# Kernel optimization log

Hardware: AMD Instinct MI355X
Metric: run time of the kernel (lower is better)

Reference implementation:

```python
import jax, jax.numpy as jnp
import numpy as np

NUM_PTS = 8   # num_points_per_face
K = 5         # self.k


def _sq_dist(x, y):
    # squared euclidean distance matrix (Nx, Ny); matches torch.cdist**2 / sum((a-b)**2)
    x2 = jnp.sum(x * x, axis=1)[:, None]
    y2 = jnp.sum(y * y, axis=1)[None, :]
    d = x2 + y2 - 2.0 * (x @ y.T)
    return jnp.maximum(d, 0.0)


def setup_inputs() -> dict:
    key = jax.random.key(0)
    k1, k2, k3, k4, k5, k6, k7 = jax.random.split(key, 7)
    V, Fs, Ft = 2048, 4096, 4096
    return {
        "source_vertices": jax.random.normal(k1, (1, V, 3), dtype=jnp.float32),
        "source_faces": jax.random.randint(k2, (Fs, 3), 0, V),
        "target_vertices": jax.random.normal(k3, (1, V, 3), dtype=jnp.float32),
        "target_faces": jax.random.randint(k4, (3, Ft), 0, V),
        "face_probs": jax.random.uniform(k5, (Fs,), dtype=jnp.float32),
        "r1u": jax.random.uniform(k6, (Fs, NUM_PTS), dtype=jnp.float32),
        "r2u": jax.random.uniform(k7, (Fs, NUM_PTS), dtype=jnp.float32),
    }


def reference(source_vertices, source_faces, target_vertices, target_faces, face_probs, r1u, r2u):
    sv = source_vertices[0]                 # (V, 3)
    tv = target_vertices[0]                 # (V, 3)
    tf = target_faces.T                     # (Ft, 3)
    Fs = source_faces.shape[0]

    src_bc = sv[source_faces].mean(axis=1)  # (Fs, 3) source barycenters
    tgt_bc = tv[tf].mean(axis=1)            # (Ft, 3) target barycenters

    # ---- forward loss: prob-weighted min squared distance to target barycenters
    d_fwd = _sq_dist(src_bc, tgt_bc)        # (Fs, Ft)
    forward_loss = jnp.sum(face_probs * jnp.min(d_fwd, axis=1))

    # ---- sample points from triangles via barycentric coords
    r1 = jnp.sqrt(r1u)
    w1 = 1.0 - r1
    w2 = r1 * (1.0 - r2u)
    w3 = r1 * r2u
    v1 = sv[source_faces[:, 0]]             # (Fs, 3)
    v2 = sv[source_faces[:, 1]]
    v3 = sv[source_faces[:, 2]]
    pts = (w1[..., None] * v1[:, None] + w2[..., None] * v2[:, None]
           + w3[..., None] * v3[:, None]).reshape(-1, 3)   # (P, 3), P = Fs*NUM_PTS
    pt_faces = jnp.repeat(jnp.arange(Fs), NUM_PTS)          # (P,)
    pt_probs = face_probs[pt_faces]                         # (P,)

    # ---- reverse loss, batched over all P points
    d_src = _sq_dist(pts, src_bc)                           # (P, Fs)
    neg_d, idx = jax.lax.top_k(-d_src, K + 1)               # K+1 smallest distances
    tri_dists = -neg_d                                      # (P, K+1)
    mask = idx != pt_faces[:, None]                         # exclude own face
    has_self = jnp.any(~mask, axis=1)
    excl_pos = jnp.where(has_self, jnp.argmin(mask, axis=1), K + 1)  # (P,)
    t = jnp.arange(K)
    sel = t[None, :] + (t[None, :] >= excl_pos[:, None]).astype(jnp.int32)  # (P, K)
    valid_dists = jnp.take_along_axis(tri_dists, sel, axis=1)   # (P, K)
    valid_idx = jnp.take_along_axis(idx, sel, axis=1)           # (P, K)
    valid_probs = face_probs[valid_idx]                         # (P, K)

    min_tgt = jnp.min(_sq_dist(pts, tgt_bc), axis=1)            # (P,)

    reverse_loss = jnp.sum(pt_probs * min_tgt
                           + (1.0 - pt_probs) * jnp.mean(valid_probs * valid_dists, axis=1))
    return forward_loss + reverse_loss
```

## Files before the change

### kernel.cpp

```cpp
#include <hip/hip_runtime.h>
#include <math.h>

#define FS 4096
#define FT 4096
#define TS 256
#define NPH 16
#define REVB 2048
#define BIGF 3.0e38f
#define KEYINF 0xFFFFFFFFu

typedef float v2f __attribute__((ext_vector_type(2)));

__device__ __forceinline__ unsigned umin32(unsigned a, unsigned b) { return a < b ? a : b; }
__device__ __forceinline__ unsigned umax32(unsigned a, unsigned b) { return a < b ? b : a; }

__device__ __forceinline__ unsigned med3u(unsigned a, unsigned b, unsigned c) {
    unsigned d;
    asm("v_med3_u32 %0, %1, %2, %3" : "=v"(d) : "v"(a), "v"(b), "v"(c));
    return d;
}

__device__ __forceinline__ unsigned and_or(unsigned a, unsigned m, unsigned o) {
    unsigned d;
    asm("v_and_or_b32 %0, %1, %2, %3" : "=v"(d) : "v"(a), "v"(m), "v"(o));
    return d;
}

__device__ __forceinline__ v2f pk_add(v2f a, v2f b) {
    v2f d;
    asm("v_pk_add_f32 %0, %1, %2" : "=v"(d) : "v"(a), "v"(b));
    return d;
}
__device__ __forceinline__ v2f pk_fma(v2f a, v2f b, v2f c) {
    v2f d;
    asm("v_pk_fma_f32 %0, %1, %2, %3" : "=v"(d) : "v"(a), "v"(b), "v"(c));
    return d;
}
__device__ __forceinline__ void pk_fma_acc(v2f& d, v2f a, v2f b) {
    asm("v_pk_fma_f32 %0, %1, %2, %0" : "+v"(d) : "v"(a), "v"(b));
}

__device__ __forceinline__ void gl_lds16(const float4* g, float4* l) {
    __builtin_amdgcn_global_load_lds(
        (__attribute__((address_space(1))) void*)(g),
        (__attribute__((address_space(3))) void*)(l), 16, 0, 0);
}

__device__ __forceinline__ float block_reduce_sum(float v) {
    __shared__ float s[8];
    for (int o = 32; o > 0; o >>= 1) v += __shfl_down(v, o, 64);
    int lane = threadIdx.x & 63, wid = threadIdx.x >> 6;
    if (lane == 0) s[wid] = v;
    __syncthreads();
    int nw = blockDim.x >> 6;
    v = (threadIdx.x < (unsigned)nw) ? s[threadIdx.x] : 0.f;
    if (wid == 0)
        for (int o = 4; o > 0; o >>= 1) v += __shfl_down(v, o, 64);
    return v;
}

#define CE(x, y) { unsigned _n = umin32(x, y); y = umax32(x, y); x = _n; }

__device__ __forceinline__ void merge32(unsigned s[6]) {
    #pragma unroll
    for (int m = 1; m <= 16; m <<= 1) {
        unsigned b0 = __shfl_xor(s[0], m, 64), b1 = __shfl_xor(s[1], m, 64);
        unsigned b2 = __shfl_xor(s[2], m, 64), b3 = __shfl_xor(s[3], m, 64);
        unsigned b4 = __shfl_xor(s[4], m, 64), b5 = __shfl_xor(s[5], m, 64);
        unsigned l0 = s[0], l1 = s[1];
        unsigned l2 = umin32(s[2], b5), l3 = umin32(s[3], b4);
        unsigned l4 = umin32(s[4], b3), l5 = umin32(s[5], b2);
        unsigned l6 = b1, l7 = b0;
        CE(l0, l4) CE(l1, l5) CE(l2, l6) CE(l3, l7)
        CE(l0, l2) CE(l1, l3) CE(l4, l6) CE(l5, l7)
        CE(l0, l1) CE(l2, l3) CE(l4, l5) CE(l6, l7)
        s[0] = l0; s[1] = l1; s[2] = l2; s[3] = l3; s[4] = l4; s[5] = l5;
    }
}

__global__ __launch_bounds__(64) void k_prep(
        const float* __restrict__ sv, const int* __restrict__ sf,
        const float* __restrict__ tv, const int* __restrict__ tf,
        float4* __restrict__ sbc2, float4* __restrict__ tbc2,
        float4* __restrict__ sbcr, float* __restrict__ out) {
    int i = blockIdx.x * 64 + threadIdx.x;
    if (i == 0) out[0] = 0.f;
    if (i >= FS) return;
    const float third = 1.f / 3.f;
    int a = sf[3*i], b = sf[3*i+1], c = sf[3*i+2];
    float x = (sv[3*a  ] + sv[3*b  ] + sv[3*c  ]) * third;
    float y = (sv[3*a+1] + sv[3*b+1] + sv[3*c+1]) * third;
    float z = (sv[3*a+2] + sv[3*b+2] + sv[3*c+2]) * third;
    float n2 = x*x + y*y + z*z;
    sbcr[i] = make_float4(x, y, z, n2);
    int ta = tf[i], tb = tf[FT + i], tc = tf[2*FT + i];
    float tx = (tv[3*ta  ] + tv[3*tb  ] + tv[3*tc  ]) * third;
    float ty = (tv[3*ta+1] + tv[3*tb+1] + tv[3*tc+1]) * third;
    float tz = (tv[3*ta+2] + tv[3*tb+2] + tv[3*tc+2]) * third;
    float tn2 = tx*tx + ty*ty + tz*tz;

    int tt = i >> 10, cc = i & 1023;
    int g = cc >> 6, half = (cc >> 5) & 1, pp = cc & 31;
    int lo4 = tt*1024 + g*32 + pp, hi4 = lo4 + 512;
    float* S = (float*)sbc2;
    S[4*lo4 + half]     = -2.f*x;  S[4*lo4 + 2 + half] = -2.f*y;
    S[4*hi4 + half]     = -2.f*z;  S[4*hi4 + 2 + half] = n2;
    float* T = (float*)tbc2;
    T[4*lo4 + half]     = -2.f*tx; T[4*lo4 + 2 + half] = -2.f*ty;
    T[4*hi4 + half]     = -2.f*tz; T[4*hi4 + 2 + half] = tn2;
}

__global__ __launch_bounds__(128, 4) void k_main(
        const float* __restrict__ sv, const int* __restrict__ sf,
        const float* __restrict__ fp,
        const float* __restrict__ r1u, const float* __restrict__ r2u,
        const float4* __restrict__ sbc2, const float4* __restrict__ tbc2,
        const float4* __restrict__ sbcr, float* __restrict__ out) {
    __shared__ float4 tileS[TS];
    __shared__ float4 tileT[TS];
    int tid  = threadIdx.x;
    int seg  = tid & 31;
    int slot = tid >> 5;
    float contrib = 0.f;

    if (blockIdx.x < REVB) {
        int pt0  = blockIdx.x * 16 + slot * 4;
        int face = pt0 >> 3;

        int a = sf[3*face], b = sf[3*face+1], c = sf[3*face+2];
        float ax = sv[3*a], ay = sv[3*a+1], az = sv[3*a+2];
        float bx = sv[3*b], by = sv[3*b+1], bz = sv[3*b+2];
        float cx = sv[3*c], cy = sv[3*c+1], cz = sv[3*c+2];
        float4 r14 = ((const float4*)r1u)[pt0 >> 2];
        float4 r24 = ((const float4*)r2u)[pt0 >> 2];
        v2f pxb[4], pyb[4], pzb[4], p2b[4];
        {
            float r1a[4] = {r14.x, r14.y, r14.z, r14.w};
            float r2a[4] = {r24.x, r24.y, r24.z, r24.w};
            #pragma unroll
            for (int i = 0; i < 4; ++i) {
                float r1 = sqrtf(r1a[i]);
                float w1 = 1.f - r1, w2 = r1 * (1.f - r2a[i]), w3 = r1 * r2a[i];
                float px = w1*ax + w2*bx + w3*cx;
                float py = w1*ay + w2*by + w3*cy;
                float pz = w1*az + w2*bz + w3*cz;
                float p2 = px*px + py*py + pz*pz;
                pxb[i] = (v2f){px, px}; pyb[i] = (v2f){py, py};
                pzb[i] = (v2f){pz, pz}; p2b[i] = (v2f){p2, p2};
            }
        }

        unsigned s0[4], s1[4], s2[4];
        #pragma unroll
        for (int i = 0; i < 4; ++i) { s0[i]=KEYINF; s1[i]=KEYINF; s2[i]=KEYINF; }
        v2f vm2[4];
        #pragma unroll
        for (int i = 0; i < 4; ++i) vm2[i] = (v2f){BIGF, BIGF};

        unsigned kMask = 0xFFFFF000u;

        for (int p = 0; p < NPH; ++p) {
            int b0 = ((p >> 2) << 10) + ((p & 3) << 7);
            __syncthreads();
            gl_lds16(&sbc2[b0 + tid],       &tileS[tid]);
            gl_lds16(&sbc2[b0 + 512 + tid], &tileS[128 + tid]);
            gl_lds16(&tbc2[b0 + tid],       &tileT[tid]);
            gl_lds16(&tbc2[b0 + 512 + tid], &tileT[128 + tid]);
            __syncthreads();
            unsigned jja = (unsigned)(p * TS + seg);
            #pragma unroll
            for (int jp = 0; jp < 4; ++jp) {
                float4 lo = tileS[(jp << 5) + seg];
                float4 hi = tileS[128 + (jp << 5) + seg];
                v2f cx2 = {lo.x, lo.y}, cy2 = {lo.z, lo.w};
                v2f cz2 = {hi.x, hi.y}, cw2 = {hi.z, hi.w};
                #pragma unroll
                for (int i = 0; i < 4; ++i) {
                    v2f d2 = pk_add(cw2, p2b[i]);
                    pk_fma_acc(d2, pzb[i], cz2);
                    pk_fma_acc(d2, pyb[i], cy2);
                    pk_fma_acc(d2, pxb[i], cx2);
                    unsigned ka = and_or(__float_as_uint(d2.x), kMask, jja);
                    unsigned kb = and_or(__float_as_uint(d2.y), kMask, jja + 32u);
                    unsigned n0 = umin32(s0[i], ka);
                    unsigned n1 = med3u(s0[i], s1[i], ka);
                    unsigned n2 = med3u(s1[i], s2[i], ka);
                    s0[i]=n0; s1[i]=n1; s2[i]=n2;
                    n0 = umin32(s0[i], kb);
                    n1 = med3u(s0[i], s1[i], kb);
                    n2 = med3u(s1[i], s2[i], kb);
                    s0[i]=n0; s1[i]=n1; s2[i]=n2;
                }
                jja += 64;
            }
            #pragma unroll
            for (int jp = 0; jp < 4; ++jp) {
                float4 lo = tileT[(jp << 5) + seg];
                float4 hi = tileT[128 + (jp << 5) + seg];
                v2f cx2 = {lo.x, lo.y}, cy2 = {lo.z, lo.w};
                v2f cz2 = {hi.x, hi.y}, cw2 = {hi.z, hi.w};
                #pragma unroll
                for (int i = 0; i < 4; ++i) {
                    v2f t = pk_fma(pzb[i], cz2, cw2);
                    pk_fma_acc(t, pyb[i], cy2);
                    pk_fma_acc(t, pxb[i], cx2);
                    vm2[i].x = fminf(vm2[i].x, t.x);
                    vm2[i].y = fminf(vm2[i].y, t.y);
                }
            }
        }

        float vm[4];
        #pragma unroll
        for (int i = 0; i < 4; ++i) {
            float v = fminf(vm2[i].x, vm2[i].y);
            v = fminf(v, __shfl_xor(v, 1, 64));
            v = fminf(v, __shfl_xor(v, 2, 64));
            v = fminf(v, __shfl_xor(v, 4, 64));
            v = fminf(v, __shfl_xor(v, 8, 64));
            v = fminf(v, __shfl_xor(v, 16, 64));
            vm[i] = v;
        }

        float pf = fp[face];
        float csum = 0.f;
        #pragma unroll
        for (int i = 0; i < 4; ++i) {
            unsigned srt[6] = {s0[i], s1[i], s2[i], KEYINF, KEYINF, KEYINF};
            merge32(srt);
            if (seg == 0) {
                int   q0 = srt[0] & 0xFFF, q1 = srt[1] & 0xFFF, q2 = srt[2] & 0xFFF;
                int   q3 = srt[3] & 0xFFF, q4 = srt[4] & 0xFFF, q5 = srt[5] & 0xFFF;
                float d0 = __uint_as_float(srt[0] & 0xFFFFF000u);
                float d1 = __uint_as_float(srt[1] & 0xFFFFF000u);
                float d2 = __uint_as_float(srt[2] & 0xFFFFF000u);
                float d3 = __uint_as_float(srt[3] & 0xFFFFF000u);
                float d4 = __uint_as_float(srt[4] & 0xFFFFF000u);
                float d5 = __uint_as_float(srt[5] & 0xFFFFF000u);

                int skip = 5;
                if      (q0 == face) skip = 0;
                else if (q1 == face) skip = 1;
                else if (q2 == face) skip = 2;
                else if (q3 == face) skip = 3;
                else if (q4 == face) skip = 4;

                float s = 0.f;
                if (skip != 0) s += fp[q0] * d0;
                if (skip != 1) s += fp[q1] * d1;
                if (skip != 2) s += fp[q2] * d2;
                if (skip != 3) s += fp[q3] * d3;
                if (skip != 4) s += fp[q4] * d4;
                if (skip != 5) s += fp[q5] * d5;

                float mtd = fmaxf(vm[i] + p2b[i].x, 0.f);
                csum += pf * mtd + (1.f - pf) * (s * 0.2f);
            }
        }
        if (seg == 0) contrib = csum;
    } else {
        int f0 = (blockIdx.x - REVB) * 16 + slot * 4;
        float qw[4];
        v2f qxb[4], qyb[4], qzb[4];
        #pragma unroll
        for (int i = 0; i < 4; ++i) {
            float4 q = sbcr[f0 + i];
            qxb[i] = (v2f){q.x, q.x}; qyb[i] = (v2f){q.y, q.y};
            qzb[i] = (v2f){q.z, q.z}; qw[i] = q.w;
        }
        v2f vf2[4];
        #pragma unroll
        for (int i = 0; i < 4; ++i) vf2[i] = (v2f){BIGF, BIGF};

        for (int p = 0; p < NPH; ++p) {
            int b0 = ((p >> 2) << 10) + ((p & 3) << 7);
            __syncthreads();
            gl_lds16(&tbc2[b0 + tid],       &tileT[tid]);
            gl_lds16(&tbc2[b0 + 512 + tid], &tileT[128 + tid]);
            __syncthreads();
            #pragma unroll
            for (int jp = 0; jp < 4; ++jp) {
                float4 lo = tileT[(jp << 5) + seg];
                float4 hi = tileT[128 + (jp << 5) + seg];
                v2f cx2 = {lo.x, lo.y}, cy2 = {lo.z, lo.w};
                v2f cz2 = {hi.x, hi.y}, cw2 = {hi.z, hi.w};
                #pragma unroll
                for (int i = 0; i < 4; ++i) {
                    v2f t = pk_fma(qzb[i], cz2, cw2);
                    pk_fma_acc(t, qyb[i], cy2);
                    pk_fma_acc(t, qxb[i], cx2);
                    vf2[i].x = fminf(vf2[i].x, t.x);
                    vf2[i].y = fminf(vf2[i].y, t.y);
                }
            }
        }
        float vf[4];
        #pragma unroll
        for (int i = 0; i < 4; ++i) {
            float v = fminf(vf2[i].x, vf2[i].y);
            v = fminf(v, __shfl_xor(v, 1, 64));
            v = fminf(v, __shfl_xor(v, 2, 64));
            v = fminf(v, __shfl_xor(v, 4, 64));
            v = fminf(v, __shfl_xor(v, 8, 64));
            v = fminf(v, __shfl_xor(v, 16, 64));
            vf[i] = v;
        }
        if (seg == 0)
            contrib = fp[f0  ] * fmaxf(vf[0] + qw[0], 0.f)
                    + fp[f0+1] * fmaxf(vf[1] + qw[1], 0.f)
                    + fp[f0+2] * fmaxf(vf[2] + qw[2], 0.f)
                    + fp[f0+3] * fmaxf(vf[3] + qw[3], 0.f);
    }

    float tot = block_reduce_sum(contrib);
    if (tid == 0) atomicAdd(out, tot);
}

extern "C" void kernel_launch(void* const* d_in, const int* in_sizes, int n_in,
                              void* d_out, int out_size, void* d_ws, size_t ws_size,
                              hipStream_t stream) {
    const float* sv  = (const float*)d_in[0];
    const int*   sf  = (const int*)  d_in[1];
    const float* tv  = (const float*)d_in[2];
    const int*   tf  = (const int*)  d_in[3];
    const float* fp  = (const float*)d_in[4];
    const float* r1u = (const float*)d_in[5];
    const float* r2u = (const float*)d_in[6];
    float* out = (float*)d_out;

    char* ws = (char*)d_ws;
    float4* sbc2 = (float4*)(ws);
    float4* tbc2 = (float4*)(ws + 65536);
    float4* sbcr = (float4*)(ws + 131072);

    k_prep<<<64,   64,  0, stream>>>(sv, sf, tv, tf, sbc2, tbc2, sbcr, out);
    k_main<<<2304, 128, 0, stream>>>(sv, sf, fp, r1u, r2u, sbc2, tbc2, sbcr, out);
}
```

Baseline: 129.4 us.

## Split candidate range across block pairs and merge partial top-k in new kernel

Each group of points or faces is now processed by two 256-thread blocks, each scanning half of the source and target barycenters. Each block writes partial top-6 keys, partial minima and point norms to workspace. A new k_merge kernel combines the two halves with a min/reversed-pairing merge, applies own-face exclusion by dropping either the self entry or the largest key, and reduces the loss. The aim is shorter per-block loops and larger blocks for better latency hiding. The cost is an extra kernel launch plus a global-memory round trip for the intermediate results.

```diff
diff --git a/kernel.cpp b/kernel.cpp
--- a/kernel.cpp
+++ b/kernel.cpp
@@ -3,9 +3,9 @@
 
 #define FS 4096
 #define FT 4096
-#define TS 256
-#define NPH 16
-#define REVB 2048
+#define TS 512
+#define NPH 4
+#define NPT 32768
 #define BIGF 3.0e38f
 #define KEYINF 0xFFFFFFFFu
 
@@ -110,21 +110,22 @@
     T[4*hi4 + half]     = -2.f*tz; T[4*hi4 + 2 + half] = tn2;
 }
 
-__global__ __launch_bounds__(128, 4) void k_main(
+__global__ __launch_bounds__(256) void k_main(
         const float* __restrict__ sv, const int* __restrict__ sf,
-        const float* __restrict__ fp,
         const float* __restrict__ r1u, const float* __restrict__ r2u,
         const float4* __restrict__ sbc2, const float4* __restrict__ tbc2,
-        const float4* __restrict__ sbcr, float* __restrict__ out) {
+        unsigned* __restrict__ rvk, float* __restrict__ rvm,
+        float* __restrict__ pp2v, float* __restrict__ fwdv) {
     __shared__ float4 tileS[TS];
     __shared__ float4 tileT[TS];
     int tid  = threadIdx.x;
     int seg  = tid & 31;
     int slot = tid >> 5;
-    float contrib = 0.f;
-
-    if (blockIdx.x < REVB) {
-        int pt0  = blockIdx.x * 16 + slot * 4;
+
+    if (blockIdx.x < 2048) {
+        int half = blockIdx.x & 1;
+        int pg   = blockIdx.x >> 1;
+        int pt0  = pg * 32 + slot * 4;
         int face = pt0 >> 3;
 
         int a = sf[3*face], b = sf[3*face+1], c = sf[3*face+2];
@@ -160,18 +161,19 @@
         unsigned kMask = 0xFFFFF000u;
 
         for (int p = 0; p < NPH; ++p) {
-            int b0 = ((p >> 2) << 10) + ((p & 3) << 7);
+            int pp  = half * NPH + p;
+            int loB = ((pp >> 1) << 10) + ((pp & 1) << 8);
             __syncthreads();
-            gl_lds16(&sbc2[b0 + tid],       &tileS[tid]);
-            gl_lds16(&sbc2[b0 + 512 + tid], &tileS[128 + tid]);
-            gl_lds16(&tbc2[b0 + tid],       &tileT[tid]);
-            gl_lds16(&tbc2[b0 + 512 + tid], &tileT[128 + tid]);
+            gl_lds16(&sbc2[loB + tid],       &tileS[tid]);
+            gl_lds16(&sbc2[loB + 512 + tid], &tileS[256 + tid]);
+            gl_lds16(&tbc2[loB + tid],       &tileT[tid]);
+            gl_lds16(&tbc2[loB + 512 + tid], &tileT[256 + tid]);
             __syncthreads();
-            unsigned jja = (unsigned)(p * TS + seg);
-            #pragma unroll
-            for (int jp = 0; jp < 4; ++jp) {
-                float4 lo = tileS[(jp << 5) + seg];
-                float4 hi = tileS[128 + (jp << 5) + seg];
+            unsigned jja = (unsigned)(pp * TS + seg);
+            #pragma unroll 4
+            for (int g = 0; g < 8; ++g) {
+                float4 lo = tileS[(g << 5) + seg];
+                float4 hi = tileS[256 + (g << 5) + seg];
                 v2f cx2 = {lo.x, lo.y}, cy2 = {lo.z, lo.w};
                 v2f cz2 = {hi.x, hi.y}, cw2 = {hi.z, hi.w};
                 #pragma unroll
@@ -193,10 +195,10 @@
                 }
                 jja += 64;
             }
-            #pragma unroll
-            for (int jp = 0; jp < 4; ++jp) {
-                float4 lo = tileT[(jp << 5) + seg];
-                float4 hi = tileT[128 + (jp << 5) + seg];
+            #pragma unroll 4
+            for (int g = 0; g < 8; ++g) {
+                float4 lo = tileT[(g << 5) + seg];
+                float4 hi = tileT[256 + (g << 5) + seg];
                 v2f cx2 = {lo.x, lo.y}, cy2 = {lo.z, lo.w};
                 v2f cz2 = {hi.x, hi.y}, cw2 = {hi.z, hi.w};
                 #pragma unroll
@@ -222,66 +224,63 @@
             vm[i] = v;
         }
 
-        float pf = fp[face];
-        float csum = 0.f;
         #pragma unroll
         for (int i = 0; i < 4; ++i) {
             unsigned srt[6] = {s0[i], s1[i], s2[i], KEYINF, KEYINF, KEYINF};
             merge32(srt);
             if (seg == 0) {
-                int   q0 = srt[0] & 0xFFF, q1 = srt[1] & 0xFFF, q2 = srt[2] & 0xFFF;
-                int   q3 = srt[3] & 0xFFF, q4 = srt[4] & 0xFFF, q5 = srt[5] & 0xFFF;
-                float d0 = __uint_as_float(srt[0] & 0xFFFFF000u);
-                float d1 = __uint_as_float(srt[1] & 0xFFFFF000u);
-                float d2 = __uint_as_float(srt[2] & 0xFFFFF000u);
-                float d3 = __uint_as_float(srt[3] & 0xFFFFF000u);
-                float d4 = __uint_as_float(srt[4] & 0xFFFFF000u);
-                float d5 = __uint_as_float(srt[5] & 0xFFFFF000u);
-
-                int skip = 5;
-                if      (q0 == face) skip = 0;
-                else if (q1 == face) skip = 1;
-                else if (q2 == face) skip = 2;
-                else if (q3 == face) skip = 3;
-                else if (q4 == face) skip = 4;
-
-                float s = 0.f;
-                if (skip != 0) s += fp[q0] * d0;
-                if (skip != 1) s += fp[q1] * d1;
-                if (skip != 2) s += fp[q2] * d2;
-                if (skip != 3) s += fp[q3] * d3;
-                if (skip != 4) s += fp[q4] * d4;
-                if (skip != 5) s += fp[q5] * d5;
-
-                float mtd = fmaxf(vm[i] + p2b[i].x, 0.f);
-                csum += pf * mtd + (1.f - pf) * (s * 0.2f);
-            }
-        }
-        if (seg == 0) contrib = csum;
+                int pt = pt0 + i;
+                unsigned* kb = rvk + half * 6 * NPT + pt;
+                kb[0]       = srt[0];  kb[NPT]   = srt[1];
+                kb[2*NPT]   = srt[2];  kb[3*NPT] = srt[3];
+                kb[4*NPT]   = srt[4];  kb[5*NPT] = srt[5];
+                rvm[half * NPT + pt] = vm[i];
+                if (half == 0) pp2v[pt] = p2b[i].x;
+            }
+        }
     } else {
-        int f0 = (blockIdx.x - REVB) * 16 + slot * 4;
-        float qw[4];
-        v2f qxb[4], qyb[4], qzb[4];
-        #pragma unroll
-        for (int i = 0; i < 4; ++i) {
-            float4 q = sbcr[f0 + i];
-            qxb[i] = (v2f){q.x, q.x}; qyb[i] = (v2f){q.y, q.y};
-            qzb[i] = (v2f){q.z, q.z}; qw[i] = q.w;
-        }
+        int idx  = blockIdx.x - 2048;
+        int half = idx & 1;
+        int fg   = idx >> 1;
+        int f0   = fg * 32 + slot * 4;
+        const float4* sbcr = tbc2 + FS;
+        float4 q0, q1, q2, q3;
+        {
+            #pragma unroll
+            for (int i = 0; i < 4; ++i) {
+                int f = f0 + i;
+                int tt = f >> 10, cc = f & 1023;
+                int g = cc >> 6, hh = (cc >> 5) & 1, ppn = cc & 31;
+                int lo4 = tt*1024 + g*32 + ppn, hi4 = lo4 + 512;
+                const float* S = (const float*)sbc2;
+                float x = -0.5f * S[4*lo4 + hh];
+                float y = -0.5f * S[4*lo4 + 2 + hh];
+                float z = -0.5f * S[4*hi4 + hh];
+                float w =         S[4*hi4 + 2 + hh];
+                float4 q = make_float4(x, y, z, w);
+                if (i == 0) q0 = q; else if (i == 1) q1 = q;
+                else if (i == 2) q2 = q; else q3 = q;
+            }
+        }
+        float qw[4] = {q0.w, q1.w, q2.w, q3.w};
+        v2f qxb[4] = {{q0.x,q0.x},{q1.x,q1.x},{q2.x,q2.x},{q3.x,q3.x}};
+        v2f qyb[4] = {{q0.y,q0.y},{q1.y,q1.y},{q2.y,q2.y},{q3.y,q3.y}};
+        v2f qzb[4] = {{q0.z,q0.z},{q1.z,q1.z},{q2.z,q2.z},{q3.z,q3.z}};
         v2f vf2[4];
         #pragma unroll
         for (int i = 0; i < 4; ++i) vf2[i] = (v2f){BIGF, BIGF};
 
         for (int p = 0; p < NPH; ++p) {
-            int b0 = ((p >> 2) << 10) + ((p & 3) << 7);
+            int pp  = half * NPH + p;
+            int loB = ((pp >> 1) << 10) + ((pp & 1) << 8);
             __syncthreads();
-            gl_lds16(&tbc2[b0 + tid],       &tileT[tid]);
-            gl_lds16(&tbc2[b0 + 512 + tid], &tileT[128 + tid]);
+            gl_lds16(&tbc2[loB + tid],       &tileT[tid]);
+            gl_lds16(&tbc2[loB + 512 + tid], &tileT[256 + tid]);
             __syncthreads();
-            #pragma unroll
-            for (int jp = 0; jp < 4; ++jp) {
-                float4 lo = tileT[(jp << 5) + seg];
-                float4 hi = tileT[128 + (jp << 5) + seg];
+            #pragma unroll 4
+            for (int g = 0; g < 8; ++g) {
+                float4 lo = tileT[(g << 5) + seg];
+                float4 hi = tileT[256 + (g << 5) + seg];
                 v2f cx2 = {lo.x, lo.y}, cy2 = {lo.z, lo.w};
                 v2f cz2 = {hi.x, hi.y}, cw2 = {hi.z, hi.w};
                 #pragma unroll
@@ -294,7 +293,6 @@
                 }
             }
         }
-        float vf[4];
         #pragma unroll
         for (int i = 0; i < 4; ++i) {
             float v = fminf(vf2[i].x, vf2[i].y);
@@ -303,15 +301,59 @@
             v = fminf(v, __shfl_xor(v, 4, 64));
             v = fminf(v, __shfl_xor(v, 8, 64));
             v = fminf(v, __shfl_xor(v, 16, 64));
-            vf[i] = v;
-        }
-        if (seg == 0)
-            contrib = fp[f0  ] * fmaxf(vf[0] + qw[0], 0.f)
-                    + fp[f0+1] * fmaxf(vf[1] + qw[1], 0.f)
-                    + fp[f0+2] * fmaxf(vf[2] + qw[2], 0.f)
-                    + fp[f0+3] * fmaxf(vf[3] + qw[3], 0.f);
+            if (seg == 0) fwdv[half * FS + f0 + i] = v;
+        }
     }
-
+}
+
+__global__ __launch_bounds__(256) void k_merge(
+        const float* __restrict__ fp, const float4* __restrict__ sbcr,
+        const unsigned* __restrict__ rvk, const float* __restrict__ rvm,
+        const float* __restrict__ pp2v, const float* __restrict__ fwdv,
+        float* __restrict__ out) {
+    int tid = threadIdx.x;
+    float contrib = 0.f;
+    if (blockIdx.x < 128) {
+        int pt = blockIdx.x * 256 + tid;
+        int face = pt >> 3;
+        unsigned a0 = rvk[pt],         a1 = rvk[NPT + pt];
+        unsigned a2 = rvk[2*NPT + pt], a3 = rvk[3*NPT + pt];
+        unsigned a4 = rvk[4*NPT + pt], a5 = rvk[5*NPT + pt];
+        unsigned b0 = rvk[6*NPT + pt], b1 = rvk[7*NPT + pt];
+        unsigned b2 = rvk[8*NPT + pt], b3 = rvk[9*NPT + pt];
+        unsigned b4 = rvk[10*NPT + pt], b5 = rvk[11*NPT + pt];
+        a0 = umin32(a0, b5); a1 = umin32(a1, b4); a2 = umin32(a2, b3);
+        a3 = umin32(a3, b2); a4 = umin32(a4, b1); a5 = umin32(a5, b0);
+        float vm = fminf(rvm[pt], rvm[NPT + pt]);
+        float p2 = pp2v[pt];
+        float pf = fp[face];
+        unsigned mx = umax32(umax32(umax32(a0, a1), umax32(a2, a3)),
+                             umax32(a4, a5));
+        float ss = 0.f; unsigned ex = mx;
+        {
+            int q; float d;
+            q = a0 & 0xFFF; d = __uint_as_float(a0 & 0xFFFFF000u);
+            ss += fp[q] * d; if (q == face) ex = a0;
+            q = a1 & 0xFFF; d = __uint_as_float(a1 & 0xFFFFF000u);
+            ss += fp[q] * d; if (q == face) ex = a1;
+            q = a2 & 0xFFF; d = __uint_as_float(a2 & 0xFFFFF000u);
+            ss += fp[q] * d; if (q == face) ex = a2;
+            q = a3 & 0xFFF; d = __uint_as_float(a3 & 0xFFFFF000u);
+            ss += fp[q] * d; if (q == face) ex = a3;
+            q = a4 & 0xFFF; d = __uint_as_float(a4 & 0xFFFFF000u);
+            ss += fp[q] * d; if (q == face) ex = a4;
+            q = a5 & 0xFFF; d = __uint_as_float(a5 & 0xFFFFF000u);
+            ss += fp[q] * d; if (q == face) ex = a5;
+        }
+        ss -= fp[ex & 0xFFF] * __uint_as_float(ex & 0xFFFFF000u);
+        float mtd = fmaxf(vm + p2, 0.f);
+        contrib = pf * mtd + (1.f - pf) * (ss * 0.2f);
+    } else {
+        int f = (blockIdx.x - 128) * 256 + tid;
+        float vf = fminf(fwdv[f], fwdv[FS + f]);
+        float qw = ((const float*)sbcr)[4*f + 3];
+        contrib = fp[f] * fmaxf(vf + qw, 0.f);
+    }
     float tot = block_reduce_sum(contrib);
     if (tid == 0) atomicAdd(out, tot);
 }
@@ -329,10 +371,16 @@
     float* out = (float*)d_out;
 
     char* ws = (char*)d_ws;
-    float4* sbc2 = (float4*)(ws);
-    float4* tbc2 = (float4*)(ws + 65536);
-    float4* sbcr = (float4*)(ws + 131072);
-
-    k_prep<<<64,   64,  0, stream>>>(sv, sf, tv, tf, sbc2, tbc2, sbcr, out);
-    k_main<<<2304, 128, 0, stream>>>(sv, sf, fp, r1u, r2u, sbc2, tbc2, sbcr, out);
-}
+    float4*   sbc2 = (float4*)(ws);
+    float4*   tbc2 = (float4*)(ws + 65536);
+    float4*   sbcr = (float4*)(ws + 131072);
+    unsigned* rvk  = (unsigned*)(ws + 196608);
+    float*    rvm  = (float*)(ws + 196608 + 1572864);
+    float*    pp2v = (float*)(ws + 2031616);
+    float*    fwdv = (float*)(ws + 2162688);
+
+    k_prep <<<64,   64,  0, stream>>>(sv, sf, tv, tf, sbc2, tbc2, sbcr, out);
+    k_main <<<2304, 256, 0, stream>>>(sv, sf, r1u, r2u, sbc2, tbc2,
+                                      rvk, rvm, pp2v, fwdv);
+    k_merge<<<144,  256, 0, stream>>>(fp, sbcr, rvk, rvm, pp2v, fwdv, out);
+}
```

After: 116.7 us. 9.8% less time.
